# Kernel optimization log

Hardware: AMD Instinct MI355X
Metric: run time of the kernel (lower is better)

Reference implementation:

```python
import jax, jax.numpy as jnp
import numpy as np

B, S, HID = 2, 2048, 1024
H, KV, D = 16, 8, 64
NDIM = 2          # position_ids.shape[-1]
EPS = 1e-6
SCALING = 1.0


def _rms_norm(x, w=None, eps=EPS):
    # matches _RMSNorm: fp32 compute, optional learnable scale
    xf = x.astype(jnp.float32)
    n = xf * jax.lax.rsqrt(jnp.mean(xf * xf, axis=-1, keepdims=True) + eps)
    if w is not None:
        n = n * w.astype(jnp.float32)
    return n.astype(x.dtype)


def _rotate_half(x):
    d = x.shape[-1] // 2
    return jnp.concatenate([-x[..., d:], x[..., :d]], axis=-1)


def _apply_multidim_rope(x, cos, sin, ndim):
    # x: [B,S,h,D]; cos/sin: [B,S,D]; unsqueeze_dim=2 broadcasts over heads
    num_channels = x.shape[-1]
    cpd = 2 * (num_channels // (2 * ndim))  # channels per RoPE dimension
    outs = []
    for k in range(ndim):
        sl = slice(k * cpd, (k + 1) * cpd)
        xk = x[..., sl]
        ck = cos[..., sl][:, :, None, :]
        sk = sin[..., sl][:, :, None, :]
        outs.append(xk * ck + _rotate_half(xk) * sk)
    return jnp.concatenate(outs, axis=-1)


def setup_inputs() -> dict:
    key = jax.random.key(0)
    ks = jax.random.split(key, 10)
    scale = 0.02
    return {
        "hidden_states": jax.random.normal(ks[0], (B, S, HID), jnp.float32),
        "cos": jax.random.normal(ks[1], (B, S, D), jnp.float32),
        "sin": jax.random.normal(ks[2], (B, S, D), jnp.float32),
        "position_ids": jax.random.randint(ks[3], (B, S, NDIM), 0, 64, jnp.int64),
        "Wq": jax.random.normal(ks[4], (HID, H * D), jnp.float32) * scale,
        "Wk": jax.random.normal(ks[5], (HID, KV * D), jnp.float32) * scale,
        "Wv": jax.random.normal(ks[6], (HID, KV * D), jnp.float32) * scale,
        "Wo": jax.random.normal(ks[7], (H * D, HID), jnp.float32) * scale,
        "q_norm_w": jnp.ones((D,), jnp.float32),
        "k_norm_w": jnp.ones((D,), jnp.float32),
    }


def reference(hidden_states, cos, sin, position_ids, Wq, Wk, Wv, Wo, q_norm_w, k_norm_w):
    ndim = position_ids.shape[-1]
    bsz, seq_len, _ = hidden_states.shape

    q = (hidden_states @ Wq).reshape(bsz, seq_len, H, D)
    q = _rms_norm(q, q_norm_w)
    q = _apply_multidim_rope(q, cos, sin, ndim)
    q = jnp.transpose(q, (0, 2, 1, 3))  # [B,H,S,D]

    k = (hidden_states @ Wk).reshape(bsz, seq_len, KV, D)
    k = _rms_norm(k, k_norm_w)
    k = _apply_multidim_rope(k, cos, sin, ndim)
    k = jnp.transpose(k, (0, 2, 1, 3))  # [B,KV,S,D]

    v = (hidden_states @ Wv).reshape(bsz, seq_len, KV, D)
    v = _rms_norm(v, None)  # v_norm has no scale
    v = jnp.transpose(v, (0, 2, 1, 3))  # [B,KV,S,D]

    groups = H // KV
    if groups > 1:
        k = jnp.repeat(k, groups, axis=1)  # [B,H,S,D]
        v = jnp.repeat(v, groups, axis=1)

    scores = jnp.einsum("bhqd,bhkd->bhqk", q, k) * SCALING
    attn = jax.nn.softmax(scores.astype(jnp.float32), axis=-1).astype(q.dtype)
    out = jnp.einsum("bhqk,bhkd->bhqd", attn, v)
    out = jnp.transpose(out, (0, 2, 1, 3)).reshape(bsz, seq_len, H * D)
    return out @ Wo
```

## Files before the change

kernel.cpp:

```cpp
#include <hip/hip_runtime.h>

#define PB 2
#define PS 2048
#define PHID 1024
#define PH 16
#define PKV 8
#define PD 64
#define PM (PB*PS)
#define PR (PB*PH*PS)

typedef _Float16 f16_t;
typedef _Float16 f16x8 __attribute__((ext_vector_type(8)));
typedef _Float16 f16x2 __attribute__((ext_vector_type(2)));
typedef float f32x4 __attribute__((ext_vector_type(4)));

#define MFMAH(a,b,c)  __builtin_amdgcn_mfma_f32_16x16x32_f16((a),(b),(c),0,0,0)
#define LOG2E 1.44269504f

__device__ __forceinline__ void gl16(const f16_t* g, f16_t* l) {
  __builtin_amdgcn_global_load_lds(
      (const __attribute__((address_space(1))) void*)g,
      (__attribute__((address_space(3))) void*)l, 16, 0, 0);
}

__global__ __launch_bounds__(256)
void convert_hs(const float* __restrict__ hs, f16_t* __restrict__ hf)
{
  const size_t i = ((size_t)blockIdx.x * 256 + threadIdx.x) * 8;
  float4 a = *(const float4*)&hs[i];
  float4 b = *(const float4*)&hs[i + 4];
  float xs[8] = {a.x, a.y, a.z, a.w, b.x, b.y, b.z, b.w};
  f16x8 v;
  #pragma unroll
  for (int j = 0; j < 8; ++j) v[j] = (f16_t)xs[j];
  *(f16x8*)&hf[i] = v;
}

__global__ __launch_bounds__(256)
void convert_w(const float* __restrict__ Wq, const float* __restrict__ Wk,
               const float* __restrict__ Wv, const float* __restrict__ Wo,
               f16_t* __restrict__ wtT)
{
  __shared__ float Tt[64][68];
  const int tid = threadIdx.x;
  const int slot = blockIdx.x >> 4, k0 = (blockIdx.x & 15) * 64;

  const float* src; int N, ncol0, orow0;
  if (slot < 16)      { src = Wq; N = 1024; ncol0 = slot*64;      orow0 = slot*64; }
  else if (slot < 24) { src = Wk; N = 512;  ncol0 = (slot-16)*64; orow0 = 1024 + (slot-16)*64; }
  else if (slot < 32) { src = Wv; N = 512;  ncol0 = (slot-24)*64; orow0 = 1536 + (slot-24)*64; }
  else                { src = Wo; N = 1024; ncol0 = (slot-32)*64; orow0 = 2048 + (slot-32)*64; }

  const int tk = tid >> 6, tn = tid & 63;
  #pragma unroll
  for (int i = 0; i < 16; ++i)
    Tt[tn][tk*16 + i] = src[(size_t)(k0 + tk*16 + i) * N + ncol0 + tn];
  __syncthreads();

  const int n = tid >> 2, kc = (tid & 3) * 16;
  f16x8 a0, a1;
  #pragma unroll
  for (int i = 0; i < 8; ++i) {
    a0[i] = (f16_t)Tt[n][kc + i];
    a1[i] = (f16_t)Tt[n][kc + 8 + i];
  }
  const size_t ob = (size_t)(orow0 + n) * 1024 + k0 + kc;
  *(f16x8*)&wtT[ob]     = a0;
  *(f16x8*)&wtT[ob + 8] = a1;
}

__global__ __launch_bounds__(256)
void qkv_kernel(const f16_t* __restrict__ hsf, const f16_t* __restrict__ wtT,
                const float* __restrict__ cosp, const float* __restrict__ sinp,
                const float* __restrict__ qnw, const float* __restrict__ knw,
                f16_t* __restrict__ q_o, f16_t* __restrict__ k_o,
                f16_t* __restrict__ vt_o)
{
  __shared__ __align__(16) f16_t Ah[128][64];
  __shared__ __align__(16) f16_t Bh[128][64];

  const int tid = threadIdx.x;
  const int lane = tid & 63, wave = tid >> 6;
  const int lo16 = lane & 15, hi4 = lane >> 4;
  const int lin = blockIdx.x;
  const int swz = (lin & 7) * 64 + (lin >> 3);
  const int m0 = (swz >> 4) * 128;
  const int ws = swz & 15;
  const int orow = ws * 128;

  int kind, hd0;
  if (ws < 8)       { kind = 0; hd0 = ws*2; }
  else if (ws < 12) { kind = 1; hd0 = (ws-8)*2; }
  else              { kind = 2; hd0 = (ws-12)*2; }

  f32x4 acc[2][8];
  #pragma unroll
  for (int qb = 0; qb < 2; ++qb)
    #pragma unroll
    for (int j = 0; j < 8; ++j) acc[qb][j] = f32x4{0.f, 0.f, 0.f, 0.f};

  const int ri = lane >> 3, pc = lane & 7;
  const int lcs = (pc ^ ri) * 8;
  size_t aoff4[4]; f16_t* aldst4[4];
  size_t boff4[4]; f16_t* bldst4[4];
  #pragma unroll
  for (int q = 0; q < 4; ++q) {
    aoff4[q] = (size_t)(m0 + wave*32 + q*8 + ri) * PHID + lcs;
    aldst4[q] = &Ah[wave*32 + q*8][0];
    boff4[q] = (size_t)(orow + wave*32 + q*8 + ri) * 1024 + lcs;
    bldst4[q] = &Bh[wave*32 + q*8][0];
  }

  const int rsw = lo16 & 7;

  for (int k0 = 0; k0 < PHID; k0 += 64) {
    __syncthreads();
    #pragma unroll
    for (int q = 0; q < 4; ++q) gl16(hsf + aoff4[q] + k0, aldst4[q]);
    #pragma unroll
    for (int q = 0; q < 4; ++q) gl16(wtT + boff4[q] + k0, bldst4[q]);
    __syncthreads();

    #pragma unroll
    for (int t = 0; t < 2; ++t) {
      const int ccol = ((t*4 + hi4) ^ rsw) * 8;
      f16x8 ah[2];
      #pragma unroll
      for (int qb = 0; qb < 2; ++qb)
        ah[qb] = *(const f16x8*)&Ah[wave*32 + qb*16 + lo16][ccol];
      #pragma unroll
      for (int j = 0; j < 8; ++j) {
        f16x8 bh = *(const f16x8*)&Bh[j*16 + lo16][ccol];
        #pragma unroll
        for (int qb = 0; qb < 2; ++qb)
          acc[qb][j] = MFMAH(ah[qb], bh, acc[qb][j]);
      }
    }
  }

  float nwv[4];
  #pragma unroll
  for (int jj = 0; jj < 4; ++jj)
    nwv[jj] = (kind == 0) ? qnw[lo16 + 16*jj]
            : (kind == 1) ? knw[lo16 + 16*jj] : 1.0f;

  #pragma unroll
  for (int qb = 0; qb < 2; ++qb) {
    float sc[2][4];
    #pragma unroll
    for (int r = 0; r < 4; ++r) {
      float s0 = 0.f, s1 = 0.f;
      #pragma unroll
      for (int j = 0; j < 4; ++j) {
        s0 += acc[qb][j][r]   * acc[qb][j][r];
        s1 += acc[qb][j+4][r] * acc[qb][j+4][r];
      }
      #pragma unroll
      for (int m = 1; m < 16; m <<= 1) {
        s0 += __shfl_xor(s0, m);
        s1 += __shfl_xor(s1, m);
      }
      sc[0][r] = 1.0f / sqrtf(s0 * (1.0f/64.0f) + 1e-6f);
      sc[1][r] = 1.0f / sqrtf(s1 * (1.0f/64.0f) + 1e-6f);
    }

    float y[8][4];
    #pragma unroll
    for (int j = 0; j < 8; ++j)
      #pragma unroll
      for (int r = 0; r < 4; ++r)
        y[j][r] = acc[qb][j][r] * sc[j>>2][r] * nwv[j&3];

    if (kind == 2) {
      #pragma unroll
      for (int r = 0; r < 4; ++r) {
        int mg = m0 + wave*32 + qb*16 + hi4*4 + r;
        int b = mg >> 11, sq = mg & 2047;
        int g = sq & 63;
        int sp = (g & 3) | (((g >> 4) & 1) << 2) | (((g >> 2) & 1) << 3)
               | (((g >> 3) & 1) << 4) | (g & 32);
        int sq2 = (sq & ~63) | sp;
        #pragma unroll
        for (int j = 0; j < 8; ++j) {
          int d = lo16 + 16*(j & 3), hd = hd0 + (j >> 2);
          vt_o[((size_t)((b*PKV + hd)*PD + d))*PS + sq2] = (f16_t)y[j][r];
        }
      }
    } else {
      #pragma unroll
      for (int r = 0; r < 4; ++r) {
        int mg = m0 + wave*32 + qb*16 + hi4*4 + r;
        int b = mg >> 11, sq = mg & 2047;
        const float* cp = &cosp[(size_t)mg * PD];
        const float* sp = &sinp[(size_t)mg * PD];
        float z[8];
        #pragma unroll
        for (int j = 0; j < 8; ++j) {
          int d = lo16 + 16*(j & 3);
          float c = cp[d], s = sp[d];
          float rot = (j & 1) ? y[j-1][r] : -y[j+1][r];
          z[j] = y[j][r] * c + rot * s;
        }
        #pragma unroll
        for (int j = 0; j < 8; ++j) {
          int d = lo16 + 16*(j & 3), hd = hd0 + (j >> 2);
          if (kind == 0) {
            size_t idx = ((size_t)(b*PH + hd)*PS + sq)*PD + d;
            q_o[idx] = (f16_t)(z[j] * LOG2E);
          } else {
            size_t idx = ((size_t)(b*PKV + hd)*PS + sq)*PD + d;
            k_o[idx] = (f16_t)z[j];
          }
        }
      }
    }
  }
}

__global__ __launch_bounds__(256, 4)
void attn_kernel(const f16_t* __restrict__ q_g, const f16_t* __restrict__ k_g,
                 const f16_t* __restrict__ vt_g,
                 f16_t* __restrict__ op, float2* __restrict__ ml)
{
  __shared__ __align__(16) char lds_raw[32768];
  f16_t (*Ks)[64][64] = (f16_t (*)[64][64])lds_raw;
  f16_t (*Vs)[64][64] = (f16_t (*)[64][64])(lds_raw + 16384);
  f16_t (*Ob)[72]     = (f16_t (*)[72])lds_raw;

  const int tid = threadIdx.x, lane = tid & 63, wave = tid >> 6;
  const int lo16 = lane & 15, hi4 = lane >> 4;
  const int lin = blockIdx.x;
  const int swz = (lin & 7) * 128 + (lin >> 3);
  const int qt = swz & 15;
  const int bh = (swz >> 4) & 31;
  const int ks = swz >> 9;
  const int b = bh >> 4, h = bh & 15, kvh = h >> 1;

  f16x8 qf[2][2];
  #pragma unroll
  for (int qb = 0; qb < 2; ++qb) {
    const size_t qbase = ((size_t)(b*PH + h)*PS + qt*128 + wave*32 + qb*16 + lo16) * PD;
    #pragma unroll
    for (int t = 0; t < 2; ++t)
      qf[qb][t] = *(const f16x8*)&q_g[qbase + t*32 + hi4*8];
  }

  f32x4 o[2][4];
  float mq[2] = {-1e30f, -1e30f}, lq[2] = {0.f, 0.f};
  #pragma unroll
  for (int qb = 0; qb < 2; ++qb)
    #pragma unroll
    for (int j = 0; j < 4; ++j) o[qb][j] = f32x4{0.f, 0.f, 0.f, 0.f};

  const f32x4 FZ = {0.f, 0.f, 0.f, 0.f};

  const int ri = lane >> 3;
  const int lcs = ((lane & 7) ^ ri) * 8;
  const size_t kbase = (size_t)(b*PKV + kvh) * PS * PD + (size_t)ks * 1024 * PD;
  const size_t vbase = (size_t)(b*PKV + kvh) * PD * PS + (size_t)ks * 1024;

  auto STAGE = [&](int kt, int buf) {
    const f16_t* kp = k_g + kbase + (size_t)kt * 64 * PD;
    const f16_t* vp = vt_g + vbase + kt * 64;
    #pragma unroll
    for (int i = 0; i < 2; ++i) {
      const int st = wave*2 + i;
      gl16(kp + (st*8 + ri)*PD + lcs, &Ks[buf][st*8][0]);
      gl16(vp + (size_t)(st*8 + ri)*PS + lcs, &Vs[buf][st*8][0]);
    }
  };

  STAGE(0, 0);
  int cur = 0;
  const int rsw = lo16 & 7;

  for (int kt = 0; kt < 16; ++kt) {
    __syncthreads();
    if (kt + 1 < 16) STAGE(kt + 1, cur ^ 1);

    f32x4 sacc[2][4];
    __builtin_amdgcn_s_setprio(1);
    #pragma unroll
    for (int j = 0; j < 4; ++j) {
      f16x8 kf0 = *(const f16x8*)&Ks[cur][j*16 + lo16][(hi4 ^ rsw) * 8];
      f16x8 kf1 = *(const f16x8*)&Ks[cur][j*16 + lo16][((4 + hi4) ^ rsw) * 8];
      #pragma unroll
      for (int qb = 0; qb < 2; ++qb)
        sacc[qb][j] = MFMAH(kf1, qf[qb][1], MFMAH(kf0, qf[qb][0], FZ));
    }
    __builtin_amdgcn_s_setprio(0);

    f16x8 pa[2][2];
    #pragma unroll
    for (int qb = 0; qb < 2; ++qb) {
      float x0 = fmaxf(fmaxf(sacc[qb][0][0], sacc[qb][0][1]),
                       fmaxf(sacc[qb][0][2], sacc[qb][0][3]));
      float x1 = fmaxf(fmaxf(sacc[qb][1][0], sacc[qb][1][1]),
                       fmaxf(sacc[qb][1][2], sacc[qb][1][3]));
      float x2 = fmaxf(fmaxf(sacc[qb][2][0], sacc[qb][2][1]),
                       fmaxf(sacc[qb][2][2], sacc[qb][2][3]));
      float x3 = fmaxf(fmaxf(sacc[qb][3][0], sacc[qb][3][1]),
                       fmaxf(sacc[qb][3][2], sacc[qb][3][3]));
      float tm = fmaxf(fmaxf(x0, x1), fmaxf(x2, x3));
      tm = fmaxf(tm, __shfl_xor(tm, 16));
      tm = fmaxf(tm, __shfl_xor(tm, 32));
      if (!__all(tm <= mq[qb] + 8.0f)) {
        float mnew = fmaxf(mq[qb], tm);
        float alpha = __builtin_amdgcn_exp2f(mq[qb] - mnew);
        lq[qb] *= alpha;
        #pragma unroll
        for (int jd = 0; jd < 4; ++jd) o[qb][jd] *= alpha;
        mq[qb] = mnew;
      }
      float ls = 0.f;
      #pragma unroll
      for (int t = 0; t < 2; ++t) {
        f16x8 v;
        #pragma unroll
        for (int e = 0; e < 8; ++e) {
          float p = __builtin_amdgcn_exp2f(sacc[qb][2*t + (e >> 2)][e & 3] - mq[qb]);
          ls += p;
          v[e] = (f16_t)p;
        }
        pa[qb][t] = v;
      }
      ls += __shfl_xor(ls, 16);
      ls += __shfl_xor(ls, 32);
      lq[qb] += ls;
    }

    __builtin_amdgcn_s_setprio(1);
    #pragma unroll
    for (int jd = 0; jd < 4; ++jd) {
      #pragma unroll
      for (int t = 0; t < 2; ++t) {
        f16x8 vf = *(const f16x8*)&Vs[cur][jd*16 + lo16][((t*4 + hi4) ^ rsw) * 8];
        #pragma unroll
        for (int qb = 0; qb < 2; ++qb)
          o[qb][jd] = MFMAH(vf, pa[qb][t], o[qb][jd]);
      }
    }
    __builtin_amdgcn_s_setprio(0);

    cur ^= 1;
  }

  __syncthreads();
  const int rbase = bh*PS + qt*128 + wave*32;
  if (hi4 == 0) {
    #pragma unroll
    for (int qb = 0; qb < 2; ++qb)
      ml[(size_t)ks*PR + rbase + qb*16 + lo16] = float2{mq[qb], lq[qb]};
  }
  #pragma unroll
  for (int qb = 0; qb < 2; ++qb) {
    float inv = 1.0f / lq[qb];
    #pragma unroll
    for (int jd = 0; jd < 4; ++jd)
      #pragma unroll
      for (int rp = 0; rp < 2; ++rp)
        *(f16x2*)&Ob[wave*32 + qb*16 + lo16][jd*16 + hi4*4 + 2*rp] =
            f16x2{(f16_t)(o[qb][jd][2*rp] * inv), (f16_t)(o[qb][jd][2*rp+1] * inv)};
  }
  {
    const int row = lane >> 1, half = lane & 1;
    const size_t gb_ = ((size_t)ks*PR + rbase + row) * PD + half*32;
    #pragma unroll
    for (int c = 0; c < 4; ++c)
      *(f16x8*)&op[gb_ + c*8] = *(const f16x8*)&Ob[wave*32 + row][half*32 + c*8];
  }
}

__global__ __launch_bounds__(256)
void merge_kernel(const f16_t* __restrict__ op, const float2* __restrict__ ml,
                  f16_t* __restrict__ ao)
{
  const int gid = blockIdx.x * 256 + threadIdx.x;
  const int row = gid >> 3, oct = gid & 7;
  float2 e0 = ml[row], e1 = ml[PR + row];
  float M = fmaxf(e0.x, e1.x);
  float c0 = __builtin_amdgcn_exp2f(e0.x - M) * e0.y;
  float c1 = __builtin_amdgcn_exp2f(e1.x - M) * e1.y;
  float inv = 1.0f / (c0 + c1);
  c0 *= inv; c1 *= inv;
  f16x8 a = *(const f16x8*)&op[(size_t)row*PD + oct*8];
  f16x8 bq = *(const f16x8*)&op[(size_t)(PR + row)*PD + oct*8];
  f16x8 r;
  #pragma unroll
  for (int i = 0; i < 8; ++i)
    r[i] = (f16_t)(c0 * (float)a[i] + c1 * (float)bq[i]);
  const int bh = row >> 11, sq = row & 2047;
  const int b = bh >> 4, h = bh & 15;
  *(f16x8*)&ao[((size_t)(b*PS + sq))*PHID + h*PD + oct*8] = r;
}

__global__ __launch_bounds__(256)
void oproj_kernel(const f16_t* __restrict__ ao, const f16_t* __restrict__ woT,
                  float* __restrict__ out)
{
  __shared__ __align__(16) f16_t As[128][40], Bs[64][40];
  const int tid = threadIdx.x;
  const int lane = tid & 63, wave = tid >> 6;
  const int lo16 = lane & 15, hi4 = lane >> 4;
  const int lin = blockIdx.x;
  const int swz = (lin & 7) * 64 + (lin >> 3);
  const int m0 = (swz >> 4) * 128;
  const int col0 = (swz & 15) * 64;

  f32x4 acc[2][4];
  #pragma unroll
  for (int qb = 0; qb < 2; ++qb)
    #pragma unroll
    for (int j = 0; j < 4; ++j) acc[qb][j] = f32x4{0.f, 0.f, 0.f, 0.f};

  const int ar = tid >> 1, akc = (tid & 1) * 16;
  const int bn = tid & 63, bkc = (tid >> 6) * 8;

  f16x8 gA0, gA1, gB;
  auto LOADA = [&](int k0) {
    const f16_t* ap = &ao[(size_t)(m0 + ar) * PHID + k0 + akc];
    gA0 = *(const f16x8*)ap;
    gA1 = *(const f16x8*)(ap + 8);
  };
  auto LOADB = [&](int k0) {
    gB = *(const f16x8*)&woT[(size_t)(col0 + bn) * 1024 + k0 + bkc];
  };
  LOADA(0); LOADB(0);

  for (int k0 = 0; k0 < PHID; k0 += 32) {
    __syncthreads();
    *(f16x8*)&As[ar][akc]     = gA0;
    *(f16x8*)&As[ar][akc + 8] = gA1;
    *(f16x8*)&Bs[bn][bkc]     = gB;
    if (k0 + 32 < PHID) { LOADA(k0 + 32); LOADB(k0 + 32); }
    __syncthreads();
    {
      f16x8 a[2];
      #pragma unroll
      for (int qb = 0; qb < 2; ++qb)
        a[qb] = *(const f16x8*)&As[wave*32 + qb*16 + lo16][hi4*8];
      #pragma unroll
      for (int j = 0; j < 4; ++j) {
        f16x8 bb = *(const f16x8*)&Bs[j*16 + lo16][hi4*8];
        #pragma unroll
        for (int qb = 0; qb < 2; ++qb)
          acc[qb][j] = MFMAH(a[qb], bb, acc[qb][j]);
      }
    }
  }

  #pragma unroll
  for (int qb = 0; qb < 2; ++qb)
    #pragma unroll
    for (int r = 0; r < 4; ++r) {
      int mg = m0 + wave*32 + qb*16 + hi4*4 + r;
      #pragma unroll
      for (int j = 0; j < 4; ++j)
        out[(size_t)mg*PHID + col0 + lo16 + 16*j] = acc[qb][j][r];
    }
}

extern "C" void kernel_launch(void* const* d_in, const int* in_sizes, int n_in,
                              void* d_out, int out_size, void* d_ws, size_t ws_size,
                              hipStream_t stream) {
  (void)in_sizes; (void)n_in; (void)out_size; (void)ws_size;
  const float* hs   = (const float*)d_in[0];
  const float* cosp = (const float*)d_in[1];
  const float* sinp = (const float*)d_in[2];
  const float* Wq   = (const float*)d_in[4];
  const float* Wk   = (const float*)d_in[5];
  const float* Wv   = (const float*)d_in[6];
  const float* Wo   = (const float*)d_in[7];
  const float* qnw  = (const float*)d_in[8];
  const float* knw  = (const float*)d_in[9];
  float* out = (float*)d_out;

  const size_t QN = (size_t)PB*PH*PS*PD;
  const size_t KN = (size_t)PB*PKV*PS*PD;
  const size_t HN = (size_t)PM*PHID;
  char* wsb = (char*)d_ws;
  f16_t*  qv  = (f16_t*)wsb;
  f16_t*  kv  = qv + QN;
  f16_t*  vt  = kv + KN;
  f16_t*  hsf = vt + KN;
  f16_t*  wtT = hsf + HN;
  f16_t*  op  = wtT + (size_t)3072*1024;
  float2* ml  = (float2*)(op + 2*QN);
  f16_t*  ao  = qv;
  const f16_t* woT = wtT + (size_t)2048*1024;

  convert_hs<<<dim3(2048), 256, 0, stream>>>(hs, hsf);
  convert_w <<<dim3(768),  256, 0, stream>>>(Wq, Wk, Wv, Wo, wtT);
  qkv_kernel<<<dim3(512),  256, 0, stream>>>(hsf, wtT, cosp, sinp,
                                             qnw, knw, qv, kv, vt);
  attn_kernel<<<dim3(1024), 256, 0, stream>>>(qv, kv, vt, op, ml);
  merge_kernel<<<dim3(PR*8/256), 256, 0, stream>>>(op, ml, ao);
  oproj_kernel<<<dim3(512), 256, 0, stream>>>(ao, woT, out);
}
```

Before: 119.2 us.

## Fold max subtraction into MFMA accumulator and compute row sums via MFMA

The softmax inner loop now seeds the QK^T MFMA accumulator with -m, so the running max is subtracted inside the matrix op instead of per element. The row sum is accumulated by an extra MFMA against a ones vector rather than scalar adds and cross-lane shuffles. Probabilities are packed with cvt_pkrtz, and the occupancy hint drops from 4 to 3 waves per SIMD to allow more registers. This trades VALU and shuffle work for extra MFMA issue slots, a larger register footprint, and round-toward-zero conversion of probabilities.

Result: no change. 118.7 us (-0.4%).

```diff
diff --git a/kernel.cpp b/kernel.cpp
--- a/kernel.cpp
+++ b/kernel.cpp
@@ -12,6 +12,7 @@
 typedef _Float16 f16_t;
 typedef _Float16 f16x8 __attribute__((ext_vector_type(8)));
 typedef _Float16 f16x2 __attribute__((ext_vector_type(2)));
+typedef __fp16 fp16v2 __attribute__((ext_vector_type(2)));
 typedef float f32x4 __attribute__((ext_vector_type(4)));
 
 #define MFMAH(a,b,c)  __builtin_amdgcn_mfma_f32_16x16x32_f16((a),(b),(c),0,0,0)
@@ -217,7 +218,7 @@
   }
 }
 
-__global__ __launch_bounds__(256, 4)
+__global__ __launch_bounds__(256, 3)
 void attn_kernel(const f16_t* __restrict__ q_g, const f16_t* __restrict__ k_g,
                  const f16_t* __restrict__ vt_g,
                  f16_t* __restrict__ op, float2* __restrict__ ml)
@@ -245,14 +246,18 @@
       qf[qb][t] = *(const f16x8*)&q_g[qbase + t*32 + hi4*8];
   }
 
-  f32x4 o[2][4];
-  float mq[2] = {-1e30f, -1e30f}, lq[2] = {0.f, 0.f};
-  #pragma unroll
-  for (int qb = 0; qb < 2; ++qb)
+  f32x4 o[2][4], lsum[2];
+  float mq[2] = {0.f, 0.f};
+  #pragma unroll
+  for (int qb = 0; qb < 2; ++qb) {
+    lsum[qb] = f32x4{0.f, 0.f, 0.f, 0.f};
     #pragma unroll
     for (int j = 0; j < 4; ++j) o[qb][j] = f32x4{0.f, 0.f, 0.f, 0.f};
-
-  const f32x4 FZ = {0.f, 0.f, 0.f, 0.f};
+  }
+
+  f16x8 ONES;
+  #pragma unroll
+  for (int e = 0; e < 8; ++e) ONES[e] = (f16_t)1.0f;
 
   const int ri = lane >> 3;
   const int lcs = ((lane & 7) ^ ri) * 8;
@@ -285,48 +290,64 @@
       f16x8 kf0 = *(const f16x8*)&Ks[cur][j*16 + lo16][(hi4 ^ rsw) * 8];
       f16x8 kf1 = *(const f16x8*)&Ks[cur][j*16 + lo16][((4 + hi4) ^ rsw) * 8];
       #pragma unroll
-      for (int qb = 0; qb < 2; ++qb)
-        sacc[qb][j] = MFMAH(kf1, qf[qb][1], MFMAH(kf0, qf[qb][0], FZ));
+      for (int qb = 0; qb < 2; ++qb) {
+        f32x4 mc = {-mq[qb], -mq[qb], -mq[qb], -mq[qb]};
+        sacc[qb][j] = MFMAH(kf1, qf[qb][1], MFMAH(kf0, qf[qb][0], mc));
+      }
     }
     __builtin_amdgcn_s_setprio(0);
 
     f16x8 pa[2][2];
     #pragma unroll
     for (int qb = 0; qb < 2; ++qb) {
-      float x0 = fmaxf(fmaxf(sacc[qb][0][0], sacc[qb][0][1]),
-                       fmaxf(sacc[qb][0][2], sacc[qb][0][3]));
-      float x1 = fmaxf(fmaxf(sacc[qb][1][0], sacc[qb][1][1]),
-                       fmaxf(sacc[qb][1][2], sacc[qb][1][3]));
-      float x2 = fmaxf(fmaxf(sacc[qb][2][0], sacc[qb][2][1]),
-                       fmaxf(sacc[qb][2][2], sacc[qb][2][3]));
-      float x3 = fmaxf(fmaxf(sacc[qb][3][0], sacc[qb][3][1]),
-                       fmaxf(sacc[qb][3][2], sacc[qb][3][3]));
-      float tm = fmaxf(fmaxf(x0, x1), fmaxf(x2, x3));
+      float m0_ = fmaxf(fmaxf(sacc[qb][0][0], sacc[qb][0][1]), sacc[qb][0][2]);
+      float m1_ = fmaxf(fmaxf(sacc[qb][0][3], sacc[qb][1][0]), sacc[qb][1][1]);
+      float m2_ = fmaxf(fmaxf(sacc[qb][1][2], sacc[qb][1][3]), sacc[qb][2][0]);
+      float m3_ = fmaxf(fmaxf(sacc[qb][2][1], sacc[qb][2][2]), sacc[qb][2][3]);
+      float m4_ = fmaxf(fmaxf(sacc[qb][3][0], sacc[qb][3][1]), sacc[qb][3][2]);
+      float tm  = fmaxf(fmaxf(m0_, m1_), m2_);
+      tm = fmaxf(fmaxf(tm, m3_), m4_);
+      tm = fmaxf(tm, sacc[qb][3][3]);
       tm = fmaxf(tm, __shfl_xor(tm, 16));
       tm = fmaxf(tm, __shfl_xor(tm, 32));
-      if (!__all(tm <= mq[qb] + 8.0f)) {
-        float mnew = fmaxf(mq[qb], tm);
-        float alpha = __builtin_amdgcn_exp2f(mq[qb] - mnew);
-        lq[qb] *= alpha;
+
+      if (!__all(tm <= 8.0f)) {
+        float tmx = fmaxf(tm, 0.f);
+        float alpha = __builtin_amdgcn_exp2f(-tmx);
+        lsum[qb] *= alpha;
         #pragma unroll
         for (int jd = 0; jd < 4; ++jd) o[qb][jd] *= alpha;
-        mq[qb] = mnew;
-      }
-      float ls = 0.f;
-      #pragma unroll
-      for (int t = 0; t < 2; ++t) {
-        f16x8 v;
-        #pragma unroll
-        for (int e = 0; e < 8; ++e) {
-          float p = __builtin_amdgcn_exp2f(sacc[qb][2*t + (e >> 2)][e & 3] - mq[qb]);
-          ls += p;
-          v[e] = (f16_t)p;
+        mq[qb] += tmx;
+        #pragma unroll
+        for (int t = 0; t < 2; ++t) {
+          union { fp16v2 h[4]; f16x8 v; } u;
+          #pragma unroll
+          for (int pr = 0; pr < 2; ++pr) {
+            float p0 = __builtin_amdgcn_exp2f(sacc[qb][2*t+pr][0] - tmx);
+            float p1 = __builtin_amdgcn_exp2f(sacc[qb][2*t+pr][1] - tmx);
+            float p2 = __builtin_amdgcn_exp2f(sacc[qb][2*t+pr][2] - tmx);
+            float p3 = __builtin_amdgcn_exp2f(sacc[qb][2*t+pr][3] - tmx);
+            u.h[pr*2]   = __builtin_amdgcn_cvt_pkrtz(p0, p1);
+            u.h[pr*2+1] = __builtin_amdgcn_cvt_pkrtz(p2, p3);
+          }
+          pa[qb][t] = u.v;
         }
-        pa[qb][t] = v;
-      }
-      ls += __shfl_xor(ls, 16);
-      ls += __shfl_xor(ls, 32);
-      lq[qb] += ls;
+      } else {
+        #pragma unroll
+        for (int t = 0; t < 2; ++t) {
+          union { fp16v2 h[4]; f16x8 v; } u;
+          #pragma unroll
+          for (int pr = 0; pr < 2; ++pr) {
+            float p0 = __builtin_amdgcn_exp2f(sacc[qb][2*t+pr][0]);
+            float p1 = __builtin_amdgcn_exp2f(sacc[qb][2*t+pr][1]);
+            float p2 = __builtin_amdgcn_exp2f(sacc[qb][2*t+pr][2]);
+            float p3 = __builtin_amdgcn_exp2f(sacc[qb][2*t+pr][3]);
+            u.h[pr*2]   = __builtin_amdgcn_cvt_pkrtz(p0, p1);
+            u.h[pr*2+1] = __builtin_amdgcn_cvt_pkrtz(p2, p3);
+          }
+          pa[qb][t] = u.v;
+        }
+      }
     }
 
     __builtin_amdgcn_s_setprio(1);
@@ -340,6 +361,11 @@
           o[qb][jd] = MFMAH(vf, pa[qb][t], o[qb][jd]);
       }
     }
+    #pragma unroll
+    for (int qb = 0; qb < 2; ++qb)
+      #pragma unroll
+      for (int t = 0; t < 2; ++t)
+        lsum[qb] = MFMAH(ONES, pa[qb][t], lsum[qb]);
     __builtin_amdgcn_s_setprio(0);
 
     cur ^= 1;
@@ -350,11 +376,11 @@
   if (hi4 == 0) {
     #pragma unroll
     for (int qb = 0; qb < 2; ++qb)
-      ml[(size_t)ks*PR + rbase + qb*16 + lo16] = float2{mq[qb], lq[qb]};
+      ml[(size_t)ks*PR + rbase + qb*16 + lo16] = float2{mq[qb], lsum[qb][0]};
   }
   #pragma unroll
   for (int qb = 0; qb < 2; ++qb) {
-    float inv = 1.0f / lq[qb];
+    float inv = 1.0f / lsum[qb][0];
     #pragma unroll
     for (int jd = 0; jd < 4; ++jd)
       #pragma unroll
```

## Load oproj tiles directly into LDS with XOR swizzle and larger K step

Applied to the files above, without the earlier changes.

The output projection GEMM now uses global_load_lds to copy A and B tiles straight into shared memory, replacing the register-staged loads and stores. An XOR swizzle on 16-byte chunks replaces row padding to avoid bank conflicts, and the K tile doubles from 32 to 64. The goal is to cut VGPR traffic, LDS write instructions and sync iterations. In exchange, the register-level prefetch of the next tile is gone, so load latency now overlaps with compute only across waves and blocks.

Result: no change. 117.5 us (-1.4%).

```diff
diff --git a/kernel.cpp b/kernel.cpp
--- a/kernel.cpp
+++ b/kernel.cpp
@@ -398,7 +398,9 @@
 void oproj_kernel(const f16_t* __restrict__ ao, const f16_t* __restrict__ woT,
                   float* __restrict__ out)
 {
-  __shared__ __align__(16) f16_t As[128][40], Bs[64][40];
+  __shared__ __align__(16) f16_t As[128][64];
+  __shared__ __align__(16) f16_t Bs[64][64];
+
   const int tid = threadIdx.x;
   const int lane = tid & 63, wave = tid >> 6;
   const int lo16 = lane & 15, hi4 = lane >> 4;
@@ -413,35 +415,41 @@
     #pragma unroll
     for (int j = 0; j < 4; ++j) acc[qb][j] = f32x4{0.f, 0.f, 0.f, 0.f};
 
-  const int ar = tid >> 1, akc = (tid & 1) * 16;
-  const int bn = tid & 63, bkc = (tid >> 6) * 8;
-
-  f16x8 gA0, gA1, gB;
-  auto LOADA = [&](int k0) {
-    const f16_t* ap = &ao[(size_t)(m0 + ar) * PHID + k0 + akc];
-    gA0 = *(const f16x8*)ap;
-    gA1 = *(const f16x8*)(ap + 8);
-  };
-  auto LOADB = [&](int k0) {
-    gB = *(const f16x8*)&woT[(size_t)(col0 + bn) * 1024 + k0 + bkc];
-  };
-  LOADA(0); LOADB(0);
-
-  for (int k0 = 0; k0 < PHID; k0 += 32) {
+  const int ri = lane >> 3, pc = lane & 7;
+  const int lcs = (pc ^ ri) * 8;
+  size_t aoff4[4]; f16_t* aldst4[4];
+  #pragma unroll
+  for (int q = 0; q < 4; ++q) {
+    aoff4[q] = (size_t)(m0 + wave*32 + q*8 + ri) * PHID + lcs;
+    aldst4[q] = &As[wave*32 + q*8][0];
+  }
+  size_t boff[2]; int brow[2];
+  #pragma unroll
+  for (int q = 0; q < 2; ++q) {
+    brow[q] = wave*16 + q*8;
+    boff[q] = (size_t)(col0 + brow[q] + ri) * 1024 + lcs;
+  }
+
+  const int rsw = lo16 & 7;
+
+  for (int k0 = 0; k0 < PHID; k0 += 64) {
     __syncthreads();
-    *(f16x8*)&As[ar][akc]     = gA0;
-    *(f16x8*)&As[ar][akc + 8] = gA1;
-    *(f16x8*)&Bs[bn][bkc]     = gB;
-    if (k0 + 32 < PHID) { LOADA(k0 + 32); LOADB(k0 + 32); }
+    #pragma unroll
+    for (int q = 0; q < 4; ++q) gl16(ao + aoff4[q] + k0, aldst4[q]);
+    #pragma unroll
+    for (int q = 0; q < 2; ++q) gl16(woT + boff[q] + k0, &Bs[brow[q]][0]);
     __syncthreads();
-    {
+
+    #pragma unroll
+    for (int t = 0; t < 2; ++t) {
+      const int ccol = ((t*4 + hi4) ^ rsw) * 8;
       f16x8 a[2];
       #pragma unroll
       for (int qb = 0; qb < 2; ++qb)
-        a[qb] = *(const f16x8*)&As[wave*32 + qb*16 + lo16][hi4*8];
+        a[qb] = *(const f16x8*)&As[wave*32 + qb*16 + lo16][ccol];
       #pragma unroll
       for (int j = 0; j < 4; ++j) {
-        f16x8 bb = *(const f16x8*)&Bs[j*16 + lo16][hi4*8];
+        f16x8 bb = *(const f16x8*)&Bs[j*16 + lo16][ccol];
         #pragma unroll
         for (int qb = 0; qb < 2; ++qb)
           acc[qb][j] = MFMAH(a[qb], bb, acc[qb][j]);
```
